# Performance work log

Hardware: AMD Instinct MI355X
Metric: run time of the kernel (lower is better)

The kernel has to match this reference:

```python
import jax, jax.numpy as jnp
import numpy as np

L2RG = 1e-4

def setup_inputs() -> dict:
    key = jax.random.key(0)
    ks = jax.random.split(key, 12)
    B, U, I, C, D = 16384, 200000, 100000, 2000, 512
    user = jax.random.randint(ks[0], (B,), 0, U)
    item = jax.random.randint(ks[1], (B,), 0, I)
    cate = jax.random.randint(ks[2], (B,), 0, C)
    rate = jax.random.uniform(ks[3], (B,), jnp.float32, 1.0, 5.0)
    # embedding tables, std=0.01, padding_idx=0 row zeroed
    user_w = (0.01 * jax.random.normal(ks[4], (U, D), jnp.float32)).at[0].set(0.0)
    item_w = (0.01 * jax.random.normal(ks[5], (I, D), jnp.float32)).at[0].set(0.0)
    cate_w = (0.01 * jax.random.normal(ks[6], (C, D), jnp.float32)).at[0].set(0.0)
    p = jax.random.uniform(ks[7], (C,), jnp.float32)
    cate_prior = p / p.sum()
    s = 1.0 / np.sqrt(D)
    w1 = jax.random.uniform(ks[8], (D, D), jnp.float32, -s, s)
    b1 = jnp.zeros((D,), jnp.float32)
    w2 = jax.random.uniform(ks[9], (D, D), jnp.float32, -s, s)
    b2 = jnp.zeros((D,), jnp.float32)
    w3 = jax.random.uniform(ks[10], (D, 1), jnp.float32, -s, s)
    b3 = jnp.zeros((1,), jnp.float32)
    return dict(user=user, item=item, cate=cate, rate=rate,
                user_w=user_w, item_w=item_w, cate_w=cate_w, cate_prior=cate_prior,
                w1=w1, b1=b1, w2=w2, b2=b2, w3=w3, b3=b3)


def reference(user, item, cate, rate, user_w, item_w, cate_w, cate_prior,
              w1, b1, w2, b2, w3, b3):
    B = user.shape[0]
    ue = user_w[user]   # [B, D]
    ie = item_w[item]   # [B, D]
    ce = cate_w[cate]   # [B, D]
    # weighted cate embeddings are batch-independent: precompute sum and sum-of-squares
    wc = cate_w * cate_prior[:, None]          # [C, D]
    cs = wc.sum(axis=0)                        # [D]
    css = (wc * wc).sum(axis=0)                # [D]
    # FM identity on concat([user_emb, weighted_cate_embs]) along field axis
    s1 = ue + cs
    q1 = ue * ue + css
    ucm = 0.5 * (s1 * s1 - q1)                 # [B, D] user-confounder mediator
    # second FM over fields [ue, ie, ce, ucm]
    s2 = ue + ie + ce + ucm
    q2 = ue * ue + ie * ie + ce * ce + ucm * ucm
    fm_out = 0.5 * (s2 * s2 - q2)              # [B, D]
    # MLP (dropout is identity in eval / p=0)
    h = jax.nn.relu(fm_out @ w1 + b1)
    h = jax.nn.relu(h @ w2 + b2)
    logits = (h @ w3 + b3)[:, 0]               # [B]
    pred = 1.0 + 4.0 * jax.nn.sigmoid(logits)  # rescale_rate=True
    rate_loss = jnp.mean((pred - rate) ** 2)
    reg = 0.5 * (jnp.sum(ue * ue) + jnp.sum(ie * ie) + jnp.sum(ce * ce))
    loss = rate_loss + L2RG * reg / B
    return loss
```

## Files before the change

### kernel.cpp

```cpp
#include <hip/hip_runtime.h>
#include <hip/hip_bf16.h>
#include <math.h>

#define B_SZ 16384
#define D_SZ 512
#define C_SZ 2000

#define ASCALE 64.f
#define WSCALE 16.f
#define HSCALE 1024.f
#define INV1 (1.f / (ASCALE * WSCALE))
#define INV2 (1.f / (HSCALE * WSCALE))

typedef float f32x4 __attribute__((ext_vector_type(4)));
typedef unsigned short ushort8 __attribute__((ext_vector_type(8)));

__device__ __forceinline__ f32x4 ntload4(const float* p) {
  return __builtin_nontemporal_load((const f32x4*)p);
}
__device__ __forceinline__ unsigned int pk4_fp8(float a, float b, float c, float d) {
  int r = __builtin_amdgcn_cvt_pk_fp8_f32(a, b, 0, false);
  r = __builtin_amdgcn_cvt_pk_fp8_f32(c, d, r, true);
  return (unsigned int)r;
}
__device__ __forceinline__ unsigned char f2fp8(float v) {
  int r = __builtin_amdgcn_cvt_pk_fp8_f32(v, 0.f, 0, false);
  return (unsigned char)(r & 0xff);
}

__global__ __launch_bounds__(256) void prep(
    const float* __restrict__ cw, const float* __restrict__ prior,
    const float* __restrict__ w1, const float* __restrict__ w2,
    float* __restrict__ cs, float* __restrict__ css,
    unsigned char* __restrict__ w1q, unsigned char* __restrict__ w2q) {
  __shared__ float ls[2][4][64];
  __shared__ float tile[64][65];
  const int t = threadIdx.x;
  int bid = blockIdx.x;
  if (bid < 128) {
    const int dl = t & 63, g = t >> 6;
    const int dchunk = bid & 7, cchunk = bid >> 3;
    const int d = (dchunk << 6) + dl;
    const int cstart = cchunk * 125, cend = cstart + 125;
    float s = 0.f, ss = 0.f;
    for (int c = cstart + g; c < cend; c += 4) {
      float w = cw[(size_t)c * D_SZ + d] * prior[c];
      s += w; ss += w * w;
    }
    ls[0][g][dl] = s; ls[1][g][dl] = ss;
    __syncthreads();
    if (t < 64) {
      atomicAdd(cs + (dchunk << 6) + t,
                ls[0][0][t] + ls[0][1][t] + ls[0][2][t] + ls[0][3][t]);
      atomicAdd(css + (dchunk << 6) + t,
                ls[1][0][t] + ls[1][1][t] + ls[1][2][t] + ls[1][3][t]);
    }
    return;
  }
  bid -= 128;
  const float* src = w1; unsigned char* dst = w1q;
  if (bid >= 64) { src = w2; dst = w2q; bid -= 64; }
  const int kt = (bid >> 3) << 6;
  const int nt = (bid & 7) << 6;
  const int r0 = t >> 4, c0 = (t & 15) << 2;
  #pragma unroll
  for (int rr = 0; rr < 4; ++rr) {
    const int r = r0 + rr * 16;
    float4 v = *(const float4*)(src + (size_t)(kt + r) * 512 + nt + c0);
    tile[r][c0] = v.x; tile[r][c0 + 1] = v.y;
    tile[r][c0 + 2] = v.z; tile[r][c0 + 3] = v.w;
  }
  __syncthreads();
  const int nr = t >> 2, kc = (t & 3) << 4;
  const int n = nt + nr;
  uint4 o;
  o.x = pk4_fp8(tile[kc + 0][nr] * WSCALE, tile[kc + 1][nr] * WSCALE,
                tile[kc + 2][nr] * WSCALE, tile[kc + 3][nr] * WSCALE);
  o.y = pk4_fp8(tile[kc + 4][nr] * WSCALE, tile[kc + 5][nr] * WSCALE,
                tile[kc + 6][nr] * WSCALE, tile[kc + 7][nr] * WSCALE);
  o.z = pk4_fp8(tile[kc + 8][nr] * WSCALE, tile[kc + 9][nr] * WSCALE,
                tile[kc + 10][nr] * WSCALE, tile[kc + 11][nr] * WSCALE);
  o.w = pk4_fp8(tile[kc + 12][nr] * WSCALE, tile[kc + 13][nr] * WSCALE,
                tile[kc + 14][nr] * WSCALE, tile[kc + 15][nr] * WSCALE);
  *(uint4*)(dst + ((size_t)((kt + kc) >> 5) << 14) + (n << 5) + (kc & 31)) = o;
}

__device__ __forceinline__ float fme(float u, float i, float c, float s, float ssq,
                                     float& reg) {
  float ucm = fmaf(u, s, 0.5f * (s * s - ssq));
  float s2 = u + i + c + ucm;
  float q2 = u * u + i * i + c * c + ucm * ucm;
  reg += u * u + i * i + c * c;
  return 0.5f * (s2 * s2 - q2);
}

__global__ __launch_bounds__(512) void mega(
    const int* __restrict__ user, const int* __restrict__ item,
    const int* __restrict__ cate, const float* __restrict__ rate,
    const float* __restrict__ uw, const float* __restrict__ iw,
    const float* __restrict__ cw, const float* __restrict__ cs,
    const float* __restrict__ css,
    const unsigned char* __restrict__ w1q, const unsigned char* __restrict__ w2q,
    const float* __restrict__ b1, const float* __restrict__ b2,
    const float* __restrict__ w3, const float* __restrict__ b3,
    float* __restrict__ accs, float* __restrict__ out) {
  __shared__ unsigned char sA[64 * 512];
  __shared__ float plog[8][68];
  __shared__ float red[8];
  const int t = threadIdx.x;
  const int lane = t & 63, w = t >> 6;
  const int r0 = blockIdx.x << 6;

  {
    const int row = t >> 3;
    const int g8 = (t & 7) << 3;
    const int b = r0 + row;
    const float* up = uw + (size_t)user[b] * D_SZ;
    const float* ip = iw + (size_t)item[b] * D_SZ;
    const float* cp = cw + (size_t)cate[b] * D_SZ;
    float regp = 0.f;
    const int aswz = (row & 7) << 3;
    #pragma unroll
    for (int j = 0; j < 8; ++j) {
      const int col = (j << 6) + g8;
      f32x4 u0 = ntload4(up + col), u1 = ntload4(up + col + 4);
      f32x4 i0 = ntload4(ip + col), i1 = ntload4(ip + col + 4);
      float4 g0 = *(const float4*)(cp + col), g1 = *(const float4*)(cp + col + 4);
      float4 s0 = *(const float4*)(cs + col), s1 = *(const float4*)(cs + col + 4);
      float4 q0 = *(const float4*)(css + col), q1 = *(const float4*)(css + col + 4);
      float o0 = fme(u0[0], i0[0], g0.x, s0.x, q0.x, regp) * ASCALE;
      float o1 = fme(u0[1], i0[1], g0.y, s0.y, q0.y, regp) * ASCALE;
      float o2 = fme(u0[2], i0[2], g0.z, s0.z, q0.z, regp) * ASCALE;
      float o3 = fme(u0[3], i0[3], g0.w, s0.w, q0.w, regp) * ASCALE;
      float o4 = fme(u1[0], i1[0], g1.x, s1.x, q1.x, regp) * ASCALE;
      float o5 = fme(u1[1], i1[1], g1.y, s1.y, q1.y, regp) * ASCALE;
      float o6 = fme(u1[2], i1[2], g1.z, s1.z, q1.z, regp) * ASCALE;
      float o7 = fme(u1[3], i1[3], g1.w, s1.w, q1.w, regp) * ASCALE;
      uint2 pv;
      pv.x = pk4_fp8(o0, o1, o2, o3);
      pv.y = pk4_fp8(o4, o5, o6, o7);
      *(uint2*)(sA + (((row << 9) + col) ^ aswz)) = pv;
    }
    #pragma unroll
    for (int off = 32; off; off >>= 1) regp += __shfl_down(regp, off);
    if (lane == 0) red[w] = regp;
  }
  __syncthreads();

  const int l15 = lane & 15;
  const int lk = (lane >> 4) << 3;
  const int swz = (l15 & 7) << 3;
  const int nw = w << 6;
  const int rbase = (lane >> 4) << 2;

  f32x4 acc[4][4];
  #pragma unroll
  for (int i = 0; i < 4; ++i)
    #pragma unroll
    for (int j = 0; j < 4; ++j) acc[i][j] = (f32x4){0.f, 0.f, 0.f, 0.f};

  for (int kt = 0; kt < 512; kt += 64) {
    #pragma unroll
    for (int ks = 0; ks < 2; ++ks) {
      const int k0 = kt + (ks << 5) + lk;
      const size_t cbase = (size_t)((kt >> 5) + ks) << 14;
      long af[4], bb[4];
      #pragma unroll
      for (int mf = 0; mf < 4; ++mf)
        af[mf] = __builtin_bit_cast(long,
            *(const uint2*)(sA + ((((mf << 4) + l15) << 9) + (k0 ^ swz))));
      #pragma unroll
      for (int nf = 0; nf < 4; ++nf)
        bb[nf] = __builtin_bit_cast(long,
            *(const uint2*)(w1q + cbase + ((nw + (nf << 4) + l15) << 5) + lk));
      __builtin_amdgcn_s_setprio(1);
      #pragma unroll
      for (int mf = 0; mf < 4; ++mf)
        #pragma unroll
        for (int nf = 0; nf < 4; ++nf)
          acc[mf][nf] = __builtin_amdgcn_mfma_f32_16x16x32_fp8_fp8(
              af[mf], bb[nf], acc[mf][nf], 0, 0, 0);
      __builtin_amdgcn_s_setprio(0);
    }
  }
  __syncthreads();

  {
    #pragma unroll
    for (int nf = 0; nf < 4; ++nf) {
      const int col = nw + (nf << 4) + l15;
      const float b1c = b1[col];
      #pragma unroll
      for (int mf = 0; mf < 4; ++mf) {
        #pragma unroll
        for (int q = 0; q < 4; ++q) {
          const int row = (mf << 4) + rbase + q;
          float v = fmaxf(fmaf(acc[mf][nf][q], INV1, b1c), 0.f) * HSCALE;
          sA[(row << 9) + (col ^ ((row & 7) << 3))] = f2fp8(v);
        }
      }
    }
  }
  #pragma unroll
  for (int i = 0; i < 4; ++i)
    #pragma unroll
    for (int j = 0; j < 4; ++j) acc[i][j] = (f32x4){0.f, 0.f, 0.f, 0.f};
  __syncthreads();

  for (int kt = 0; kt < 512; kt += 64) {
    #pragma unroll
    for (int ks = 0; ks < 2; ++ks) {
      const int k0 = kt + (ks << 5) + lk;
      const size_t cbase = (size_t)((kt >> 5) + ks) << 14;
      long af[4], bb[4];
      #pragma unroll
      for (int mf = 0; mf < 4; ++mf)
        af[mf] = __builtin_bit_cast(long,
            *(const uint2*)(sA + ((((mf << 4) + l15) << 9) + (k0 ^ swz))));
      #pragma unroll
      for (int nf = 0; nf < 4; ++nf)
        bb[nf] = __builtin_bit_cast(long,
            *(const uint2*)(w2q + cbase + ((nw + (nf << 4) + l15) << 5) + lk));
      __builtin_amdgcn_s_setprio(1);
      #pragma unroll
      for (int mf = 0; mf < 4; ++mf)
        #pragma unroll
        for (int nf = 0; nf < 4; ++nf)
          acc[mf][nf] = __builtin_amdgcn_mfma_f32_16x16x32_fp8_fp8(
              af[mf], bb[nf], acc[mf][nf], 0, 0, 0);
      __builtin_amdgcn_s_setprio(0);
    }
  }

  {
    float b2c[4], wv[4];
    #pragma unroll
    for (int nf = 0; nf < 4; ++nf) {
      const int n = nw + (nf << 4) + l15;
      b2c[nf] = b2[n];
      wv[nf] = w3[n];
    }
    #pragma unroll
    for (int mf = 0; mf < 4; ++mf) {
      #pragma unroll
      for (int q = 0; q < 4; ++q) {
        float v = 0.f;
        #pragma unroll
        for (int nf = 0; nf < 4; ++nf)
          v += fmaxf(fmaf(acc[mf][nf][q], INV2, b2c[nf]), 0.f) * wv[nf];
        v += __shfl_xor(v, 1);
        v += __shfl_xor(v, 2);
        v += __shfl_xor(v, 4);
        v += __shfl_xor(v, 8);
        if (l15 == 0) plog[w][(mf << 4) + rbase + q] = v;
      }
    }
  }
  __syncthreads();
  if (t < 64) {
    float s = 0.f;
    #pragma unroll
    for (int ww = 0; ww < 8; ++ww) s += plog[ww][t];
    float logit = s + b3[0];
    float pred = 1.f + 4.f / (1.f + expf(-logit));
    float d = pred - rate[r0 + t];
    float v = d * d;
    #pragma unroll
    for (int off = 32; off; off >>= 1) v += __shfl_down(v, off);
    if (t == 0) atomicAdd(&accs[0], v);
  } else if (t == 64) {
    atomicAdd(&accs[1], red[0] + red[1] + red[2] + red[3] +
                        red[4] + red[5] + red[6] + red[7]);
  }
  __syncthreads();
  if (t == 0) {
    __threadfence();
    unsigned int prev = atomicAdd((unsigned int*)(accs + 2), 1u);
    if (prev == 255u) {
      __threadfence();
      float l = atomicAdd(&accs[0], 0.f);
      float r = atomicAdd(&accs[1], 0.f);
      out[0] = l * (1.f / (float)B_SZ) + r * (0.5e-4f / (float)B_SZ);
    }
  }
}

extern "C" void kernel_launch(void* const* d_in, const int* in_sizes, int n_in,
                              void* d_out, int out_size, void* d_ws, size_t ws_size,
                              hipStream_t stream) {
  const int* user = (const int*)d_in[0];
  const int* item = (const int*)d_in[1];
  const int* cate = (const int*)d_in[2];
  const float* rate = (const float*)d_in[3];
  const float* uw = (const float*)d_in[4];
  const float* iw = (const float*)d_in[5];
  const float* cw = (const float*)d_in[6];
  const float* prior = (const float*)d_in[7];
  const float* w1 = (const float*)d_in[8];
  const float* b1 = (const float*)d_in[9];
  const float* w2 = (const float*)d_in[10];
  const float* b2 = (const float*)d_in[11];
  const float* w3 = (const float*)d_in[12];
  const float* b3 = (const float*)d_in[13];
  float* out = (float*)d_out;

  unsigned char* w1q = (unsigned char*)d_ws;
  unsigned char* w2q = w1q + 262144;
  float* cs   = (float*)(w2q + 262144);
  float* css  = cs + 512;
  float* accs = css + 512;

  hipMemsetAsync(cs, 0, (512 + 512 + 4) * sizeof(float), stream);
  prep<<<256, 256, 0, stream>>>(cw, prior, w1, w2, cs, css, w1q, w2q);
  mega<<<256, 512, 0, stream>>>(user, item, cate, rate, uw, iw, cw, cs, css,
                                w1q, w2q, b1, b2, w3, b3, accs, out);
}
```

Baseline: 61.88 us.

## Split embedding gather in halves and overlap second half with first GEMM

The FM embedding stage now processes only the first half of the D columns before the barrier and prefetches the user/item rows for the second half into registers. The first half of the layer-1 K loop runs on the first half of the tile while those loads are in flight, then the second half of the FM features is computed, written to shared memory, and the remaining K steps follow. The aim is to hide gather latency behind MFMA work. It also drops the s_setprio hints and simplifies weight addressing, at the cost of more live registers (64 floats of prefetch), which may lower occupancy or cause spills.

```diff
diff --git a/kernel.cpp b/kernel.cpp
--- a/kernel.cpp
+++ b/kernel.cpp
@@ -111,39 +111,42 @@
   const int lane = t & 63, w = t >> 6;
   const int r0 = blockIdx.x << 6;
 
-  {
-    const int row = t >> 3;
-    const int g8 = (t & 7) << 3;
-    const int b = r0 + row;
-    const float* up = uw + (size_t)user[b] * D_SZ;
-    const float* ip = iw + (size_t)item[b] * D_SZ;
-    const float* cp = cw + (size_t)cate[b] * D_SZ;
-    float regp = 0.f;
-    const int aswz = (row & 7) << 3;
-    #pragma unroll
-    for (int j = 0; j < 8; ++j) {
-      const int col = (j << 6) + g8;
-      f32x4 u0 = ntload4(up + col), u1 = ntload4(up + col + 4);
-      f32x4 i0 = ntload4(ip + col), i1 = ntload4(ip + col + 4);
-      float4 g0 = *(const float4*)(cp + col), g1 = *(const float4*)(cp + col + 4);
-      float4 s0 = *(const float4*)(cs + col), s1 = *(const float4*)(cs + col + 4);
-      float4 q0 = *(const float4*)(css + col), q1 = *(const float4*)(css + col + 4);
-      float o0 = fme(u0[0], i0[0], g0.x, s0.x, q0.x, regp) * ASCALE;
-      float o1 = fme(u0[1], i0[1], g0.y, s0.y, q0.y, regp) * ASCALE;
-      float o2 = fme(u0[2], i0[2], g0.z, s0.z, q0.z, regp) * ASCALE;
-      float o3 = fme(u0[3], i0[3], g0.w, s0.w, q0.w, regp) * ASCALE;
-      float o4 = fme(u1[0], i1[0], g1.x, s1.x, q1.x, regp) * ASCALE;
-      float o5 = fme(u1[1], i1[1], g1.y, s1.y, q1.y, regp) * ASCALE;
-      float o6 = fme(u1[2], i1[2], g1.z, s1.z, q1.z, regp) * ASCALE;
-      float o7 = fme(u1[3], i1[3], g1.w, s1.w, q1.w, regp) * ASCALE;
-      uint2 pv;
-      pv.x = pk4_fp8(o0, o1, o2, o3);
-      pv.y = pk4_fp8(o4, o5, o6, o7);
-      *(uint2*)(sA + (((row << 9) + col) ^ aswz)) = pv;
-    }
-    #pragma unroll
-    for (int off = 32; off; off >>= 1) regp += __shfl_down(regp, off);
-    if (lane == 0) red[w] = regp;
+  const int row = t >> 3;
+  const int g8 = (t & 7) << 3;
+  const int aswz = (row & 7) << 3;
+  const float* up = uw + (size_t)user[r0 + row] * D_SZ;
+  const float* ip = iw + (size_t)item[r0 + row] * D_SZ;
+  const float* cp = cw + (size_t)cate[r0 + row] * D_SZ;
+  float regp = 0.f;
+
+  #pragma unroll
+  for (int j = 0; j < 4; ++j) {
+    const int col = (j << 6) + g8;
+    f32x4 u0 = ntload4(up + col), u1 = ntload4(up + col + 4);
+    f32x4 i0 = ntload4(ip + col), i1 = ntload4(ip + col + 4);
+    float4 g0 = *(const float4*)(cp + col), g1 = *(const float4*)(cp + col + 4);
+    float4 s0 = *(const float4*)(cs + col), s1 = *(const float4*)(cs + col + 4);
+    float4 q0 = *(const float4*)(css + col), q1 = *(const float4*)(css + col + 4);
+    float o0 = fme(u0[0], i0[0], g0.x, s0.x, q0.x, regp) * ASCALE;
+    float o1 = fme(u0[1], i0[1], g0.y, s0.y, q0.y, regp) * ASCALE;
+    float o2 = fme(u0[2], i0[2], g0.z, s0.z, q0.z, regp) * ASCALE;
+    float o3 = fme(u0[3], i0[3], g0.w, s0.w, q0.w, regp) * ASCALE;
+    float o4 = fme(u1[0], i1[0], g1.x, s1.x, q1.x, regp) * ASCALE;
+    float o5 = fme(u1[1], i1[1], g1.y, s1.y, q1.y, regp) * ASCALE;
+    float o6 = fme(u1[2], i1[2], g1.z, s1.z, q1.z, regp) * ASCALE;
+    float o7 = fme(u1[3], i1[3], g1.w, s1.w, q1.w, regp) * ASCALE;
+    uint2 pv;
+    pv.x = pk4_fp8(o0, o1, o2, o3);
+    pv.y = pk4_fp8(o4, o5, o6, o7);
+    *(uint2*)(sA + (((row << 9) + col) ^ aswz)) = pv;
+  }
+
+  f32x4 u2[4][2], i2[4][2];
+  #pragma unroll
+  for (int j = 0; j < 4; ++j) {
+    const int col = ((j + 4) << 6) + g8;
+    u2[j][0] = ntload4(up + col); u2[j][1] = ntload4(up + col + 4);
+    i2[j][0] = ntload4(ip + col); i2[j][1] = ntload4(ip + col + 4);
   }
   __syncthreads();
 
@@ -152,12 +155,102 @@
   const int swz = (l15 & 7) << 3;
   const int nw = w << 6;
   const int rbase = (lane >> 4) << 2;
+  const int nb0 = ((nw + l15) << 5) + lk;
 
   f32x4 acc[4][4];
   #pragma unroll
   for (int i = 0; i < 4; ++i)
     #pragma unroll
     for (int j = 0; j < 4; ++j) acc[i][j] = (f32x4){0.f, 0.f, 0.f, 0.f};
+
+  #pragma unroll
+  for (int s = 0; s < 8; ++s) {
+    const int k0 = (s << 5) + lk;
+    const size_t cbase = (size_t)s << 14;
+    long af[4], bb[4];
+    #pragma unroll
+    for (int mf = 0; mf < 4; ++mf)
+      af[mf] = __builtin_bit_cast(long,
+          *(const uint2*)(sA + ((((mf << 4) + l15) << 9) + (k0 ^ swz))));
+    #pragma unroll
+    for (int nf = 0; nf < 4; ++nf)
+      bb[nf] = __builtin_bit_cast(long,
+          *(const uint2*)(w1q + cbase + nb0 + (nf << 9)));
+    #pragma unroll
+    for (int mf = 0; mf < 4; ++mf)
+      #pragma unroll
+      for (int nf = 0; nf < 4; ++nf)
+        acc[mf][nf] = __builtin_amdgcn_mfma_f32_16x16x32_fp8_fp8(
+            af[mf], bb[nf], acc[mf][nf], 0, 0, 0);
+  }
+
+  #pragma unroll
+  for (int j = 0; j < 4; ++j) {
+    const int col = ((j + 4) << 6) + g8;
+    float4 g0 = *(const float4*)(cp + col), g1 = *(const float4*)(cp + col + 4);
+    float4 s0 = *(const float4*)(cs + col), s1 = *(const float4*)(cs + col + 4);
+    float4 q0 = *(const float4*)(css + col), q1 = *(const float4*)(css + col + 4);
+    float o0 = fme(u2[j][0][0], i2[j][0][0], g0.x, s0.x, q0.x, regp) * ASCALE;
+    float o1 = fme(u2[j][0][1], i2[j][0][1], g0.y, s0.y, q0.y, regp) * ASCALE;
+    float o2 = fme(u2[j][0][2], i2[j][0][2], g0.z, s0.z, q0.z, regp) * ASCALE;
+    float o3 = fme(u2[j][0][3], i2[j][0][3], g0.w, s0.w, q0.w, regp) * ASCALE;
+    float o4 = fme(u2[j][1][0], i2[j][1][0], g1.x, s1.x, q1.x, regp) * ASCALE;
+    float o5 = fme(u2[j][1][1], i2[j][1][1], g1.y, s1.y, q1.y, regp) * ASCALE;
+    float o6 = fme(u2[j][1][2], i2[j][1][2], g1.z, s1.z, q1.z, regp) * ASCALE;
+    float o7 = fme(u2[j][1][3], i2[j][1][3], g1.w, s1.w, q1.w, regp) * ASCALE;
+    uint2 pv;
+    pv.x = pk4_fp8(o0, o1, o2, o3);
+    pv.y = pk4_fp8(o4, o5, o6, o7);
+    *(uint2*)(sA + (((row << 9) + col) ^ aswz)) = pv;
+  }
+  #pragma unroll
+  for (int off = 32; off; off >>= 1) regp += __shfl_down(regp, off);
+  if (lane == 0) red[w] = regp;
+  __syncthreads();
+
+  #pragma unroll
+  for (int s = 8; s < 16; ++s) {
+    const int k0 = (s << 5) + lk;
+    const size_t cbase = (size_t)s << 14;
+    long af[4], bb[4];
+    #pragma unroll
+    for (int mf = 0; mf < 4; ++mf)
+      af[mf] = __builtin_bit_cast(long,
+          *(const uint2*)(sA + ((((mf << 4) + l15) << 9) + (k0 ^ swz))));
+    #pragma unroll
+    for (int nf = 0; nf < 4; ++nf)
+      bb[nf] = __builtin_bit_cast(long,
+          *(const uint2*)(w1q + cbase + nb0 + (nf << 9)));
+    #pragma unroll
+    for (int mf = 0; mf < 4; ++mf)
+      #pragma unroll
+      for (int nf = 0; nf < 4; ++nf)
+        acc[mf][nf] = __builtin_amdgcn_mfma_f32_16x16x32_fp8_fp8(
+            af[mf], bb[nf], acc[mf][nf], 0, 0, 0);
+  }
+  __syncthreads();
+
+  {
+    #pragma unroll
+    for (int nf = 0; nf < 4; ++nf) {
+      const int col = nw + (nf << 4) + l15;
+      const float b1c = b1[col];
+      #pragma unroll
+      for (int mf = 0; mf < 4; ++mf) {
+        #pragma unroll
+        for (int q = 0; q < 4; ++q) {
+          const int rw = (mf << 4) + rbase + q;
+          float v = fmaxf(fmaf(acc[mf][nf][q], INV1, b1c), 0.f) * HSCALE;
+          sA[(rw << 9) + (col ^ ((rw & 7) << 3))] = f2fp8(v);
+        }
+      }
+    }
+  }
+  #pragma unroll
+  for (int i = 0; i < 4; ++i)
+    #pragma unroll
+    for (int j = 0; j < 4; ++j) acc[i][j] = (f32x4){0.f, 0.f, 0.f, 0.f};
+  __syncthreads();
 
   for (int kt = 0; kt < 512; kt += 64) {
     #pragma unroll
@@ -172,63 +265,13 @@
       #pragma unroll
       for (int nf = 0; nf < 4; ++nf)
         bb[nf] = __builtin_bit_cast(long,
-            *(const uint2*)(w1q + cbase + ((nw + (nf << 4) + l15) << 5) + lk));
-      __builtin_amdgcn_s_setprio(1);
+            *(const uint2*)(w2q + cbase + nb0 + (nf << 9)));
       #pragma unroll
       for (int mf = 0; mf < 4; ++mf)
         #pragma unroll
         for (int nf = 0; nf < 4; ++nf)
           acc[mf][nf] = __builtin_amdgcn_mfma_f32_16x16x32_fp8_fp8(
               af[mf], bb[nf], acc[mf][nf], 0, 0, 0);
-      __builtin_amdgcn_s_setprio(0);
-    }
-  }
-  __syncthreads();
-
-  {
-    #pragma unroll
-    for (int nf = 0; nf < 4; ++nf) {
-      const int col = nw + (nf << 4) + l15;
-      const float b1c = b1[col];
-      #pragma unroll
-      for (int mf = 0; mf < 4; ++mf) {
-        #pragma unroll
-        for (int q = 0; q < 4; ++q) {
-          const int row = (mf << 4) + rbase + q;
-          float v = fmaxf(fmaf(acc[mf][nf][q], INV1, b1c), 0.f) * HSCALE;
-          sA[(row << 9) + (col ^ ((row & 7) << 3))] = f2fp8(v);
-        }
-      }
-    }
-  }
-  #pragma unroll
-  for (int i = 0; i < 4; ++i)
-    #pragma unroll
-    for (int j = 0; j < 4; ++j) acc[i][j] = (f32x4){0.f, 0.f, 0.f, 0.f};
-  __syncthreads();
-
-  for (int kt = 0; kt < 512; kt += 64) {
-    #pragma unroll
-    for (int ks = 0; ks < 2; ++ks) {
-      const int k0 = kt + (ks << 5) + lk;
-      const size_t cbase = (size_t)((kt >> 5) + ks) << 14;
-      long af[4], bb[4];
-      #pragma unroll
-      for (int mf = 0; mf < 4; ++mf)
-        af[mf] = __builtin_bit_cast(long,
-            *(const uint2*)(sA + ((((mf << 4) + l15) << 9) + (k0 ^ swz))));
-      #pragma unroll
-      for (int nf = 0; nf < 4; ++nf)
-        bb[nf] = __builtin_bit_cast(long,
-            *(const uint2*)(w2q + cbase + ((nw + (nf << 4) + l15) << 5) + lk));
-      __builtin_amdgcn_s_setprio(1);
-      #pragma unroll
-      for (int mf = 0; mf < 4; ++mf)
-        #pragma unroll
-        for (int nf = 0; nf < 4; ++nf)
-          acc[mf][nf] = __builtin_amdgcn_mfma_f32_16x16x32_fp8_fp8(
-              af[mf], bb[nf], acc[mf][nf], 0, 0, 0);
-      __builtin_amdgcn_s_setprio(0);
     }
   }
 
```

Result: faster. 60.52 us (-2.2%).
